# Optimization experiments

Hardware: AMD Instinct MI355X
Metric: run time of the kernel (lower is better)

## Reference

```python
import math
import jax, jax.numpy as jnp
import numpy as np

H = 512   # hidden_size
NH = 8    # num_heads
HD = H // NH  # per_head_size


def get_embedding(max_len, dim):
    # FLAT-style sinusoidal relative position embedding over positions [-L, L-1]
    half = dim // 2
    freq = jnp.exp(jnp.arange(half, dtype=jnp.float32) * (-math.log(10000.0) / (half - 1)))
    pos = jnp.arange(-max_len, max_len, dtype=jnp.float32)  # [2L]
    ang = pos[:, None] * freq[None, :]                      # [2L, half]
    return jnp.concatenate([jnp.sin(ang), jnp.cos(ang)], axis=1)  # [2L, dim]


def setup_inputs() -> dict:
    key = jax.random.key(0)
    ks = jax.random.split(key, 9)
    B, L = 4, 1024
    return {
        "query": jax.random.normal(ks[0], (B, L, H), jnp.float32),
        "key": jax.random.normal(ks[1], (B, L, H), jnp.float32),
        "value": jax.random.normal(ks[2], (B, L, H), jnp.float32),
        "w_q_w": jax.random.normal(ks[3], (H, H), jnp.float32) * 0.02,
        "w_q_b": jnp.zeros((H,), jnp.float32),
        "w_v_w": jax.random.normal(ks[4], (H, H), jnp.float32) * 0.02,
        "w_v_b": jnp.zeros((H,), jnp.float32),
        "w_r_w": jax.random.normal(ks[5], (H, HD), jnp.float32) * 0.02,
        "w_r_b": jnp.zeros((HD,), jnp.float32),
        "r_r_bias": jax.random.normal(ks[6], (NH, HD), jnp.float32) * 0.02,
        "r_w_bias": jax.random.normal(ks[7], (NH, HD), jnp.float32) * 0.02,
        "seq_len": 1000,
    }


def reference(query, key, value, w_q_w, w_q_b, w_v_w, w_v_b, w_r_w, w_r_b,
              r_r_bias, r_w_bias, seq_len):
    B, L, _ = key.shape
    # projections (torch Linear == x @ W + b with W stored as [in, out] here)
    q = (query @ w_q_w + w_q_b).reshape(B, L, NH, HD).transpose(0, 2, 1, 3)  # [B,N,L,D]
    v = (value @ w_v_w + w_v_b).reshape(B, L, NH, HD).transpose(0, 2, 1, 3)
    k = key.reshape(B, L, NH, HD).transpose(0, 2, 1, 3)

    rel = get_embedding(L, H) @ w_r_w + w_r_b  # [2L, HD], positions -L..L-1

    rw_head_q = q + r_r_bias[None, :, None, :]
    AC = jnp.einsum('bnqd,bnkd->bnqk', rw_head_q, k)                 # [B,N,L,L]
    D_ = jnp.einsum('nd,ld->nl', r_w_bias, rel)[None, :, None, :]    # [1,N,1,2L]
    B_ = jnp.einsum('bnqd,ld->bnql', q, rel)                         # [B,N,L,2L]
    E_ = jnp.einsum('bnkd,ld->bnkl', k, rel)                         # [B,N,L,2L]
    BD = B_ + D_

    # _shift:           out[q,k] = BD[q, L + k - q]
    # _transpose_shift: out[q,k] = E_[k, L + q - k]
    qi = jnp.arange(L)
    idx_bd = L + qi[None, :] - qi[:, None]                 # [L,L]: L+k-q
    BD_sh = BD[:, :, qi[:, None], idx_bd]                  # [B,N,L,L]
    rows_e = jnp.broadcast_to(qi[None, :], (L, L))         # [L,L]: k
    idx_e = L + qi[:, None] - qi[None, :]                  # [L,L]: L+q-k
    E_sh = E_[:, :, rows_e, idx_e]                         # [B,N,L,L]

    attn = AC + BD_sh + E_sh
    mask = (jnp.arange(L) < seq_len)[None, None, None, :]  # key mask
    attn = jnp.where(mask, attn, jnp.float32(-1e15))
    attn = jax.nn.softmax(attn, axis=-1)

    out = jnp.matmul(attn, v)                               # [B,N,L,D]
    return out.transpose(0, 2, 1, 3).reshape(B, L, H)
```

## Files before the change

### kernel.cpp

```cpp
#include <hip/hip_runtime.h>
#include <math.h>

#define HDIM  512
#define NHEAD 8
#define HEADD 64
#define BATCH 4
#define SEQ   1024
#define RELN  2048
#define LOG2E 1.4426950408889634f

typedef __attribute__((ext_vector_type(8))) short s16x8;
typedef __attribute__((ext_vector_type(4))) float f32x4;

__device__ __forceinline__ unsigned short f2bf(float x) {
    unsigned u = __float_as_uint(x);
    u += 0x7fffu + ((u >> 16) & 1u);
    return (unsigned short)(u >> 16);
}
__device__ __forceinline__ float bf2f(unsigned short h) {
    return __uint_as_float(((unsigned)h) << 16);
}

__global__ __launch_bounds__(256) void rel_kernel(const float* __restrict__ w_r_w,
                                                  const float* __restrict__ w_r_b,
                                                  unsigned short* __restrict__ relbf)
{
    __shared__ float emb_s[HDIM];
    __shared__ float part[4][64];
    const int l = blockIdx.x;
    const int t = threadIdx.x;
    const float pos  = (float)(l - SEQ);
    const float coef = (float)(-9.210340371976184 / 255.0);
    {
        float fr  = expf((float)t * coef);
        float ang = pos * fr;
        emb_s[t]       = sinf(ang);
        emb_s[t + 256] = cosf(ang);
    }
    __syncthreads();
    const int d  = t & 63;
    const int ks = t >> 6;
    const float* wp = w_r_w + d;
    const int h0 = ks * 128;
    float a0 = 0.f, a1 = 0.f, a2 = 0.f, a3 = 0.f;
    #pragma unroll 8
    for (int h = 0; h < 128; h += 4) {
        a0 = fmaf(emb_s[h0 + h + 0], wp[(size_t)(h0 + h + 0) * HEADD], a0);
        a1 = fmaf(emb_s[h0 + h + 1], wp[(size_t)(h0 + h + 1) * HEADD], a1);
        a2 = fmaf(emb_s[h0 + h + 2], wp[(size_t)(h0 + h + 2) * HEADD], a2);
        a3 = fmaf(emb_s[h0 + h + 3], wp[(size_t)(h0 + h + 3) * HEADD], a3);
    }
    part[ks][d] = (a0 + a1) + (a2 + a3);
    __syncthreads();
    if (ks == 0) {
        float acc = part[0][d] + part[1][d] + part[2][d] + part[3][d] + w_r_b[d];
        relbf[(size_t)l * HEADD + d] = f2bf(acc);
    }
}

__global__ __launch_bounds__(256) void wsplit_kernel(
    const float* __restrict__ wq, const float* __restrict__ wv,
    unsigned short* __restrict__ wtq_hi, unsigned short* __restrict__ wtq_lo,
    unsigned short* __restrict__ wtv_hi, unsigned short* __restrict__ wtv_lo)
{
    __shared__ float T[64][68];
    const float* W = blockIdx.z ? wv : wq;
    unsigned short* Ohi = blockIdx.z ? wtv_hi : wtq_hi;
    unsigned short* Olo = blockIdx.z ? wtv_lo : wtq_lo;
    const int k0 = blockIdx.y * 64, n0 = blockIdx.x * 64;
    const int t = threadIdx.x;
    const int r = t >> 2, c16 = (t & 3) * 16;
    #pragma unroll
    for (int u = 0; u < 4; ++u) {
        float4 v = *(const float4*)(W + (size_t)(k0 + r) * HDIM + n0 + c16 + u * 4);
        *(float4*)&T[r][c16 + u * 4] = v;
    }
    __syncthreads();
    __align__(16) unsigned short hi[16], lo[16];
    #pragma unroll
    for (int u = 0; u < 16; ++u) {
        float x = T[c16 + u][r];
        unsigned short h = f2bf(x);
        hi[u] = h;
        lo[u] = f2bf(x - bf2f(h));
    }
    size_t base = (size_t)(n0 + r) * HDIM + k0 + c16;
    *(uint4*)(Ohi + base)     = *(uint4*)&hi[0];
    *(uint4*)(Ohi + base + 8) = *(uint4*)&hi[8];
    *(uint4*)(Olo + base)     = *(uint4*)&lo[0];
    *(uint4*)(Olo + base + 8) = *(uint4*)&lo[8];
}

__global__ void conv_bf16(const float* __restrict__ in, unsigned short* __restrict__ out, int n)
{
    int i = (blockIdx.x * 256 + threadIdx.x) * 4;
    if (i < n) {
        float4 v = *(const float4*)(in + i);
        ushort4 o;
        o.x = f2bf(v.x); o.y = f2bf(v.y); o.z = f2bf(v.z); o.w = f2bf(v.w);
        *(ushort4*)(out + i) = o;
    }
}

template<int MODE>
__global__ __launch_bounds__(256) void proj_mfma(
    const float* __restrict__ A,
    const unsigned short* __restrict__ Wt_hi,
    const unsigned short* __restrict__ Wt_lo,
    const float* __restrict__ bias,
    const float* __restrict__ e1,
    const float* __restrict__ e2,
    unsigned short* __restrict__ out1,
    unsigned short* __restrict__ out2)
{
    __shared__ unsigned short Ah[64][40], Al[64][40], Bh[64][40], Bl[64][40];
    __shared__ unsigned short Ls[64][72];
    const int t = threadIdx.x;
    const int w = t >> 6, l = t & 63, colA = l & 15, g = l >> 4, kg8 = g * 8;
    const int n0 = blockIdx.x * 64, m0 = blockIdx.y * 64;
    const int mi = w >> 1, ni = w & 1;
    const int sr = t >> 2, skc = (t & 3) * 8;
    f32x4 acc[2][2] = {};

    for (int k0 = 0; k0 < HDIM; k0 += 32) {
        {
            const float* ap = A + (size_t)(m0 + sr) * HDIM + k0 + skc;
            float4 x0 = *(const float4*)ap;
            float4 x1 = *(const float4*)(ap + 4);
            float xv[8] = {x0.x, x0.y, x0.z, x0.w, x1.x, x1.y, x1.z, x1.w};
            __align__(16) unsigned short hh[8], ll[8];
            #pragma unroll
            for (int u = 0; u < 8; ++u) {
                unsigned short h = f2bf(xv[u]);
                hh[u] = h;
                ll[u] = f2bf(xv[u] - bf2f(h));
            }
            *(uint4*)&Ah[sr][skc] = *(uint4*)hh;
            *(uint4*)&Al[sr][skc] = *(uint4*)ll;
            *(uint4*)&Bh[sr][skc] = *(const uint4*)(Wt_hi + (size_t)(n0 + sr) * HDIM + k0 + skc);
            *(uint4*)&Bl[sr][skc] = *(const uint4*)(Wt_lo + (size_t)(n0 + sr) * HDIM + k0 + skc);
        }
        __syncthreads();
        s16x8 ah[2], al[2], bh[2], bl[2];
        #pragma unroll
        for (int mt = 0; mt < 2; ++mt) {
            ah[mt] = *(const s16x8*)&Ah[mi * 32 + mt * 16 + colA][kg8];
            al[mt] = *(const s16x8*)&Al[mi * 32 + mt * 16 + colA][kg8];
        }
        #pragma unroll
        for (int nt = 0; nt < 2; ++nt) {
            bh[nt] = *(const s16x8*)&Bh[ni * 32 + nt * 16 + colA][kg8];
            bl[nt] = *(const s16x8*)&Bl[ni * 32 + nt * 16 + colA][kg8];
        }
        #pragma unroll
        for (int mt = 0; mt < 2; ++mt)
            #pragma unroll
            for (int nt = 0; nt < 2; ++nt) {
                acc[mt][nt] = __builtin_amdgcn_mfma_f32_16x16x32_bf16(al[mt], bh[nt], acc[mt][nt], 0, 0, 0);
                acc[mt][nt] = __builtin_amdgcn_mfma_f32_16x16x32_bf16(ah[mt], bl[nt], acc[mt][nt], 0, 0, 0);
                acc[mt][nt] = __builtin_amdgcn_mfma_f32_16x16x32_bf16(ah[mt], bh[nt], acc[mt][nt], 0, 0, 0);
            }
        __syncthreads();
    }

    float bv[2], ev1[2], ev2[2];
    #pragma unroll
    for (int nt = 0; nt < 2; ++nt) {
        int gn = n0 + ni * 32 + nt * 16 + colA;
        bv[nt] = bias[gn];
        if (MODE == 0) { ev1[nt] = e1[gn]; ev2[nt] = e2[gn]; }
    }

    if (MODE == 0) {
        #pragma unroll
        for (int mt = 0; mt < 2; ++mt)
            #pragma unroll
            for (int nt = 0; nt < 2; ++nt)
                #pragma unroll
                for (int rr = 0; rr < 4; ++rr)
                    Ls[mi * 32 + mt * 16 + g * 4 + rr][ni * 32 + nt * 16 + colA] =
                        f2bf(acc[mt][nt][rr] + bv[nt] + ev1[nt]);
        __syncthreads();
        {
            int r = t >> 2, c = (t & 3) * 16;
            uint4 x0 = *(uint4*)&Ls[r][c];
            uint4 x1 = *(uint4*)&Ls[r][c + 8];
            *(uint4*)(out1 + (size_t)(m0 + r) * HDIM + n0 + c)     = x0;
            *(uint4*)(out1 + (size_t)(m0 + r) * HDIM + n0 + c + 8) = x1;
        }
        __syncthreads();
        #pragma unroll
        for (int mt = 0; mt < 2; ++mt)
            #pragma unroll
            for (int nt = 0; nt < 2; ++nt)
                #pragma unroll
                for (int rr = 0; rr < 4; ++rr)
                    Ls[mi * 32 + mt * 16 + g * 4 + rr][ni * 32 + nt * 16 + colA] =
                        f2bf(acc[mt][nt][rr] + bv[nt] + ev2[nt]);
        __syncthreads();
        {
            int r = t >> 2, c = (t & 3) * 16;
            uint4 x0 = *(uint4*)&Ls[r][c];
            uint4 x1 = *(uint4*)&Ls[r][c + 8];
            *(uint4*)(out2 + (size_t)(m0 + r) * HDIM + n0 + c)     = x0;
            *(uint4*)(out2 + (size_t)(m0 + r) * HDIM + n0 + c + 8) = x1;
        }
    } else {
        #pragma unroll
        for (int mt = 0; mt < 2; ++mt)
            #pragma unroll
            for (int nt = 0; nt < 2; ++nt)
                #pragma unroll
                for (int rr = 0; rr < 4; ++rr)
                    Ls[ni * 32 + nt * 16 + colA][mi * 32 + mt * 16 + g * 4 + rr] =
                        f2bf(acc[mt][nt][rr] + bv[nt]);
        __syncthreads();
        {
            int dl = t >> 2, c = (t & 3) * 16;
            int head = n0 >> 6;
            int bb = m0 >> 10, j0 = m0 & 1023;
            uint4 x0 = *(uint4*)&Ls[dl][c];
            uint4 x1 = *(uint4*)&Ls[dl][c + 8];
            size_t vbase = ((size_t)(bb * NHEAD + head) * HEADD + dl) * SEQ + j0 + c;
            *(uint4*)(out1 + vbase)     = x0;
            *(uint4*)(out1 + vbase + 8) = x1;
        }
    }
}

__global__ __launch_bounds__(256) void flash_v3(
    const unsigned short* __restrict__ kbf,
    const unsigned short* __restrict__ qabf,
    const unsigned short* __restrict__ qbbf,
    const unsigned short* __restrict__ vT,
    const unsigned short* __restrict__ relbf,
    const int* __restrict__ seqp,
    float* __restrict__ out)
{
    __shared__ unsigned short K_s[32][72];
    __shared__ unsigned short Vt_s[64][40];
    __shared__ unsigned short R2_s[64 * 64];
    __shared__ unsigned short R3_s[64 * 64];
    __shared__ unsigned short M2t_s[64][36];
    __shared__ unsigned short M3t_s[64][36];
    __shared__ unsigned short P_s[32][40];
    __shared__ float scale_s[32];
    __shared__ float lsum_s[32];

    const int t = threadIdx.x;
    const int w = t >> 6, l = t & 63, colA = l & 15, g = l >> 4, kg8 = g * 8;
    const int i0 = blockIdx.x * 32;
    const int n = blockIdx.y, b = blockIdx.z;
    const int S = seqp[0];

    const int qa_row = i0 + (w & 1) * 16 + colA;
    const int qb_row = i0 + (w == 3 ? 16 : 0) + colA;
    const s16x8* qaP = (const s16x8*)(qabf + ((size_t)(b * SEQ + qa_row) * HDIM + n * HEADD));
    const s16x8* qbP = (const s16x8*)(qbbf + ((size_t)(b * SEQ + qb_row) * HDIM + n * HEADD));
    const s16x8 qa0 = qaP[g], qa1 = qaP[g + 4];
    const s16x8 qb0 = qbP[g], qb1 = qbP[g + 4];

    float m_run[4] = {-1e30f, -1e30f, -1e30f, -1e30f};
    float l_run[4] = {0.f, 0.f, 0.f, 0.f};
    f32x4 o0 = {0.f, 0.f, 0.f, 0.f}, o1 = {0.f, 0.f, 0.f, 0.f};

    const int krow = t >> 3, kc8 = (t & 7) * 8;
    const int vrow = t >> 2, vc8 = (t & 3) * 8;
    const int orow = (w & 1) * 16;
    const int od   = (w >> 1) * 32;

    for (int j0 = 0; j0 < S; j0 += 32) {
        *(uint4*)&K_s[krow][kc8] =
            *(const uint4*)(kbf + ((size_t)(b * SEQ + j0 + krow) * HDIM + n * HEADD + kc8));
        *(uint4*)&Vt_s[vrow][vc8] =
            *(const uint4*)(vT + ((size_t)((b * NHEAD + n) * HEADD + vrow) * SEQ + j0 + vc8));
        {
            const int base2 = SEQ + j0 - i0 - 31;
            const int base3 = SEQ + i0 - j0 - 31;
            #pragma unroll
            for (int rep = 0; rep < 2; ++rep) {
                int idx = t + rep * 256;
                if (idx < 63 * 8) {
                    int rw = idx >> 3, cc = (idx & 7) * 8;
                    unsigned swz = ((unsigned)(rw * 128 + cc * 2)) ^ (unsigned)((rw & 7) << 4);
                    *(uint4*)((char*)R2_s + swz) =
                        *(const uint4*)(relbf + (size_t)(base2 + rw) * HEADD + cc);
                    *(uint4*)((char*)R3_s + swz) =
                        *(const uint4*)(relbf + (size_t)(base3 + rw) * HEADD + cc);
                }
            }
        }
        __syncthreads();

        f32x4 accS[2] = {};
        if (w < 2) {
            #pragma unroll
            for (int ct = 0; ct < 2; ++ct) {
                s16x8 kb0 = *(const s16x8*)&K_s[ct * 16 + colA][kg8];
                s16x8 kb1 = *(const s16x8*)&K_s[ct * 16 + colA][kg8 + 32];
                accS[ct] = __builtin_amdgcn_mfma_f32_16x16x32_bf16(qa0, kb0, accS[ct], 0, 0, 0);
                accS[ct] = __builtin_amdgcn_mfma_f32_16x16x32_bf16(qa1, kb1, accS[ct], 0, 0, 0);
            }
        } else {
            const int wr = w - 2;
            s16x8 ka0 = *(const s16x8*)&K_s[wr * 16 + colA][kg8];
            s16x8 ka1 = *(const s16x8*)&K_s[wr * 16 + colA][kg8 + 32];
            #pragma unroll
            for (int ut = 0; ut < 4; ++ut) {
                int urow = ut * 16 + colA;
                unsigned sw0 = ((unsigned)(urow * 128 + kg8 * 2)) ^ (unsigned)((urow & 7) << 4);
                unsigned sw1 = ((unsigned)(urow * 128 + (kg8 + 32) * 2)) ^ (unsigned)((urow & 7) << 4);
                s16x8 rb0 = *(const s16x8*)((char*)R2_s + sw0);
                s16x8 rb1 = *(const s16x8*)((char*)R2_s + sw1);
                f32x4 c2 = {};
                c2 = __builtin_amdgcn_mfma_f32_16x16x32_bf16(qb0, rb0, c2, 0, 0, 0);
                c2 = __builtin_amdgcn_mfma_f32_16x16x32_bf16(qb1, rb1, c2, 0, 0, 0);
                ushort4 p2;
                p2.x = f2bf(c2[0]); p2.y = f2bf(c2[1]); p2.z = f2bf(c2[2]); p2.w = f2bf(c2[3]);
                *(ushort4*)&M2t_s[urow][wr * 16 + g * 4] = p2;
                s16x8 sb0 = *(const s16x8*)((char*)R3_s + sw0);
                s16x8 sb1 = *(const s16x8*)((char*)R3_s + sw1);
                f32x4 c3 = {};
                c3 = __builtin_amdgcn_mfma_f32_16x16x32_bf16(ka0, sb0, c3, 0, 0, 0);
                c3 = __builtin_amdgcn_mfma_f32_16x16x32_bf16(ka1, sb1, c3, 0, 0, 0);
                ushort4 p3;
                p3.x = f2bf(c3[0]); p3.y = f2bf(c3[1]); p3.z = f2bf(c3[2]); p3.w = f2bf(c3[3]);
                *(ushort4*)&M3t_s[urow][wr * 16 + g * 4] = p3;
            }
        }
        __syncthreads();

        if (w < 2) {
            float sv[2][4];
            #pragma unroll
            for (int ct = 0; ct < 2; ++ct) {
                int col = ct * 16 + colA;
                bool ok = (j0 + col) < S;
                #pragma unroll
                for (int rr = 0; rr < 4; ++rr) {
                    int grow = orow + g * 4 + rr;
                    float s2 = bf2f(M2t_s[col - grow + 31][grow]);
                    float s3 = bf2f(M3t_s[grow - col + 31][col]);
                    float s = accS[ct][rr] + s2 + s3;
                    sv[ct][rr] = ok ? s : -1e30f;
                }
            }
            #pragma unroll
            for (int rr = 0; rr < 4; ++rr) {
                float mm = fmaxf(sv[0][rr], sv[1][rr]);
                mm = fmaxf(mm, __shfl_xor(mm, 1));
                mm = fmaxf(mm, __shfl_xor(mm, 2));
                mm = fmaxf(mm, __shfl_xor(mm, 4));
                mm = fmaxf(mm, __shfl_xor(mm, 8));
                float mnew = fmaxf(m_run[rr], mm);
                float sc = exp2f((m_run[rr] - mnew) * LOG2E);
                m_run[rr] = mnew;
                float p0 = exp2f((sv[0][rr] - mnew) * LOG2E);
                float p1 = exp2f((sv[1][rr] - mnew) * LOG2E);
                P_s[orow + g * 4 + rr][colA]      = f2bf(p0);
                P_s[orow + g * 4 + rr][16 + colA] = f2bf(p1);
                float pp = p0 + p1;
                pp += __shfl_xor(pp, 1);
                pp += __shfl_xor(pp, 2);
                pp += __shfl_xor(pp, 4);
                pp += __shfl_xor(pp, 8);
                l_run[rr] = l_run[rr] * sc + pp;
                if (colA == 0) scale_s[orow + g * 4 + rr] = sc;
            }
        }
        __syncthreads();

        {
            float s0 = scale_s[orow + g * 4 + 0];
            float s1 = scale_s[orow + g * 4 + 1];
            float s2 = scale_s[orow + g * 4 + 2];
            float s3 = scale_s[orow + g * 4 + 3];
            o0[0] *= s0; o0[1] *= s1; o0[2] *= s2; o0[3] *= s3;
            o1[0] *= s0; o1[1] *= s1; o1[2] *= s2; o1[3] *= s3;
            s16x8 pa  = *(const s16x8*)&P_s[orow + colA][kg8];
            s16x8 vb0 = *(const s16x8*)&Vt_s[od + colA][kg8];
            s16x8 vb1 = *(const s16x8*)&Vt_s[od + 16 + colA][kg8];
            o0 = __builtin_amdgcn_mfma_f32_16x16x32_bf16(pa, vb0, o0, 0, 0, 0);
            o1 = __builtin_amdgcn_mfma_f32_16x16x32_bf16(pa, vb1, o1, 0, 0, 0);
        }
        __syncthreads();
    }

    if (w < 2 && colA == 0) {
        #pragma unroll
        for (int rr = 0; rr < 4; ++rr)
            lsum_s[orow + g * 4 + rr] = l_run[rr];
    }
    __syncthreads();
    #pragma unroll
    for (int rr = 0; rr < 4; ++rr) {
        int row = orow + g * 4 + rr;
        float inv = 1.f / lsum_s[row];
        size_t obase = (size_t)(b * SEQ + i0 + row) * HDIM + n * HEADD;
        out[obase + od + colA]      = o0[rr] * inv;
        out[obase + od + 16 + colA] = o1[rr] * inv;
    }
}

extern "C" void kernel_launch(void* const* d_in, const int* in_sizes, int n_in,
                              void* d_out, int out_size, void* d_ws, size_t ws_size,
                              hipStream_t stream) {
    (void)in_sizes; (void)n_in; (void)out_size; (void)ws_size;
    const float* query = (const float*)d_in[0];
    const float* key   = (const float*)d_in[1];
    const float* value = (const float*)d_in[2];
    const float* w_q_w = (const float*)d_in[3];
    const float* w_q_b = (const float*)d_in[4];
    const float* w_v_w = (const float*)d_in[5];
    const float* w_v_b = (const float*)d_in[6];
    const float* w_r_w = (const float*)d_in[7];
    const float* w_r_b = (const float*)d_in[8];
    const float* rrb   = (const float*)d_in[9];
    const float* rwb   = (const float*)d_in[10];
    const int*   seqp  = (const int*)d_in[11];
    float* out = (float*)d_out;

    unsigned short* wsp   = (unsigned short*)d_ws;
    const size_t NTOK = (size_t)BATCH * SEQ * HDIM;
    unsigned short* relbf  = wsp;
    unsigned short* kbf    = relbf + (size_t)RELN * HEADD;
    unsigned short* qabf   = kbf + NTOK;
    unsigned short* qbbf   = qabf + NTOK;
    unsigned short* vTbuf  = qbbf + NTOK;
    unsigned short* wtq_hi = vTbuf + NTOK;
    unsigned short* wtq_lo = wtq_hi + (size_t)HDIM * HDIM;
    unsigned short* wtv_hi = wtq_lo + (size_t)HDIM * HDIM;
    unsigned short* wtv_lo = wtv_hi + (size_t)HDIM * HDIM;

    hipLaunchKernelGGL(rel_kernel, dim3(RELN), dim3(256), 0, stream, w_r_w, w_r_b, relbf);
    hipLaunchKernelGGL(wsplit_kernel, dim3(8, 8, 2), dim3(256), 0, stream,
                       w_q_w, w_v_w, wtq_hi, wtq_lo, wtv_hi, wtv_lo);
    hipLaunchKernelGGL(conv_bf16, dim3(2048), dim3(256), 0, stream,
                       key, kbf, (int)NTOK);
    hipLaunchKernelGGL((proj_mfma<0>), dim3(8, 64), dim3(256), 0, stream,
                       query, wtq_hi, wtq_lo, w_q_b, rrb, rwb, qabf, qbbf);
    hipLaunchKernelGGL((proj_mfma<1>), dim3(8, 64), dim3(256), 0, stream,
                       value, wtv_hi, wtv_lo, w_v_b, (const float*)nullptr, (const float*)nullptr,
                       vTbuf, (unsigned short*)nullptr);
    hipLaunchKernelGGL(flash_v3, dim3(SEQ / 32, NHEAD, BATCH), dim3(256), 0, stream,
                       kbf, qabf, qbbf, vTbuf, relbf, seqp, out);
}
```

Before: 252.9 us.

## Merge prep kernels, fuse Q/V projections, read relative embeddings directly from global

The three preprocessing kernels (relative embedding, weight hi/lo split, key bf16 conversion) become one launch that dispatches on block index. The Q and V projections become one launch using blockIdx.z. In the flash kernel the shared-memory staging of the relative-embedding slices (R2_s/R3_s) is removed, and the rel-bias waves read relbf rows straight from global/L2 with clamped indices. This cuts launch overhead and shared-memory traffic and footprint, which may raise occupancy, but the flash kernel now issues uncoalesced global loads inside its inner loop.

```diff
diff --git a/kernel.cpp b/kernel.cpp
--- a/kernel.cpp
+++ b/kernel.cpp
@@ -12,6 +12,8 @@
 typedef __attribute__((ext_vector_type(8))) short s16x8;
 typedef __attribute__((ext_vector_type(4))) float f32x4;
 
+#define MFMA __builtin_amdgcn_mfma_f32_16x16x32_bf16
+
 __device__ __forceinline__ unsigned short f2bf(float x) {
     unsigned u = __float_as_uint(x);
     u += 0x7fffu + ((u >> 16) & 1u);
@@ -21,100 +23,106 @@
     return __uint_as_float(((unsigned)h) << 16);
 }
 
-__global__ __launch_bounds__(256) void rel_kernel(const float* __restrict__ w_r_w,
-                                                  const float* __restrict__ w_r_b,
-                                                  unsigned short* __restrict__ relbf)
+__global__ __launch_bounds__(256) void prep_kernel(
+    const float* __restrict__ w_r_w, const float* __restrict__ w_r_b,
+    const float* __restrict__ key,
+    const float* __restrict__ wq, const float* __restrict__ wv,
+    unsigned short* __restrict__ relbf, unsigned short* __restrict__ kbf,
+    unsigned short* __restrict__ wtq_hi, unsigned short* __restrict__ wtq_lo,
+    unsigned short* __restrict__ wtv_hi, unsigned short* __restrict__ wtv_lo)
 {
     __shared__ float emb_s[HDIM];
     __shared__ float part[4][64];
-    const int l = blockIdx.x;
+    __shared__ float T[64][68];
+    const int bid = blockIdx.x;
     const int t = threadIdx.x;
-    const float pos  = (float)(l - SEQ);
-    const float coef = (float)(-9.210340371976184 / 255.0);
-    {
-        float fr  = expf((float)t * coef);
-        float ang = pos * fr;
-        emb_s[t]       = sinf(ang);
-        emb_s[t + 256] = cosf(ang);
-    }
-    __syncthreads();
-    const int d  = t & 63;
-    const int ks = t >> 6;
-    const float* wp = w_r_w + d;
-    const int h0 = ks * 128;
-    float a0 = 0.f, a1 = 0.f, a2 = 0.f, a3 = 0.f;
-    #pragma unroll 8
-    for (int h = 0; h < 128; h += 4) {
-        a0 = fmaf(emb_s[h0 + h + 0], wp[(size_t)(h0 + h + 0) * HEADD], a0);
-        a1 = fmaf(emb_s[h0 + h + 1], wp[(size_t)(h0 + h + 1) * HEADD], a1);
-        a2 = fmaf(emb_s[h0 + h + 2], wp[(size_t)(h0 + h + 2) * HEADD], a2);
-        a3 = fmaf(emb_s[h0 + h + 3], wp[(size_t)(h0 + h + 3) * HEADD], a3);
-    }
-    part[ks][d] = (a0 + a1) + (a2 + a3);
-    __syncthreads();
-    if (ks == 0) {
-        float acc = part[0][d] + part[1][d] + part[2][d] + part[3][d] + w_r_b[d];
-        relbf[(size_t)l * HEADD + d] = f2bf(acc);
-    }
-}
-
-__global__ __launch_bounds__(256) void wsplit_kernel(
-    const float* __restrict__ wq, const float* __restrict__ wv,
-    unsigned short* __restrict__ wtq_hi, unsigned short* __restrict__ wtq_lo,
-    unsigned short* __restrict__ wtv_hi, unsigned short* __restrict__ wtv_lo)
-{
-    __shared__ float T[64][68];
-    const float* W = blockIdx.z ? wv : wq;
-    unsigned short* Ohi = blockIdx.z ? wtv_hi : wtq_hi;
-    unsigned short* Olo = blockIdx.z ? wtv_lo : wtq_lo;
-    const int k0 = blockIdx.y * 64, n0 = blockIdx.x * 64;
-    const int t = threadIdx.x;
-    const int r = t >> 2, c16 = (t & 3) * 16;
-    #pragma unroll
-    for (int u = 0; u < 4; ++u) {
-        float4 v = *(const float4*)(W + (size_t)(k0 + r) * HDIM + n0 + c16 + u * 4);
-        *(float4*)&T[r][c16 + u * 4] = v;
-    }
-    __syncthreads();
-    __align__(16) unsigned short hi[16], lo[16];
-    #pragma unroll
-    for (int u = 0; u < 16; ++u) {
-        float x = T[c16 + u][r];
-        unsigned short h = f2bf(x);
-        hi[u] = h;
-        lo[u] = f2bf(x - bf2f(h));
-    }
-    size_t base = (size_t)(n0 + r) * HDIM + k0 + c16;
-    *(uint4*)(Ohi + base)     = *(uint4*)&hi[0];
-    *(uint4*)(Ohi + base + 8) = *(uint4*)&hi[8];
-    *(uint4*)(Olo + base)     = *(uint4*)&lo[0];
-    *(uint4*)(Olo + base + 8) = *(uint4*)&lo[8];
-}
-
-__global__ void conv_bf16(const float* __restrict__ in, unsigned short* __restrict__ out, int n)
-{
-    int i = (blockIdx.x * 256 + threadIdx.x) * 4;
-    if (i < n) {
-        float4 v = *(const float4*)(in + i);
-        ushort4 o;
-        o.x = f2bf(v.x); o.y = f2bf(v.y); o.z = f2bf(v.z); o.w = f2bf(v.w);
-        *(ushort4*)(out + i) = o;
-    }
-}
-
-template<int MODE>
-__global__ __launch_bounds__(256) void proj_mfma(
-    const float* __restrict__ A,
-    const unsigned short* __restrict__ Wt_hi,
-    const unsigned short* __restrict__ Wt_lo,
-    const float* __restrict__ bias,
-    const float* __restrict__ e1,
-    const float* __restrict__ e2,
-    unsigned short* __restrict__ out1,
-    unsigned short* __restrict__ out2)
+
+    if (bid < RELN) {
+        const int l = bid;
+        const float pos  = (float)(l - SEQ);
+        const float coef = (float)(-9.210340371976184 / 255.0);
+        {
+            float fr  = expf((float)t * coef);
+            float ang = pos * fr;
+            emb_s[t]       = sinf(ang);
+            emb_s[t + 256] = cosf(ang);
+        }
+        __syncthreads();
+        const int d  = t & 63;
+        const int ks = t >> 6;
+        const float* wp = w_r_w + d;
+        const int h0 = ks * 128;
+        float a0 = 0.f, a1 = 0.f, a2 = 0.f, a3 = 0.f;
+        #pragma unroll 8
+        for (int h = 0; h < 128; h += 4) {
+            a0 = fmaf(emb_s[h0 + h + 0], wp[(size_t)(h0 + h + 0) * HEADD], a0);
+            a1 = fmaf(emb_s[h0 + h + 1], wp[(size_t)(h0 + h + 1) * HEADD], a1);
+            a2 = fmaf(emb_s[h0 + h + 2], wp[(size_t)(h0 + h + 2) * HEADD], a2);
+            a3 = fmaf(emb_s[h0 + h + 3], wp[(size_t)(h0 + h + 3) * HEADD], a3);
+        }
+        part[ks][d] = (a0 + a1) + (a2 + a3);
+        __syncthreads();
+        if (ks == 0) {
+            float acc = part[0][d] + part[1][d] + part[2][d] + part[3][d] + w_r_b[d];
+            relbf[(size_t)l * HEADD + d] = f2bf(acc);
+        }
+    } else if (bid < RELN + 128) {
+        const int idx = bid - RELN;
+        const int z = idx >> 6, rem = idx & 63;
+        const int by = rem >> 3, bx = rem & 7;
+        const float* W = z ? wv : wq;
+        unsigned short* Ohi = z ? wtv_hi : wtq_hi;
+        unsigned short* Olo = z ? wtv_lo : wtq_lo;
+        const int k0 = by * 64, n0 = bx * 64;
+        const int r = t >> 2, c16 = (t & 3) * 16;
+        #pragma unroll
+        for (int u = 0; u < 4; ++u) {
+            float4 v = *(const float4*)(W + (size_t)(k0 + r) * HDIM + n0 + c16 + u * 4);
+            *(float4*)&T[r][c16 + u * 4] = v;
+        }
+        __syncthreads();
+        __align__(16) unsigned short hi[16], lo[16];
+        #pragma unroll
+        for (int u = 0; u < 16; ++u) {
+            float x = T[c16 + u][r];
+            unsigned short h = f2bf(x);
+            hi[u] = h;
+            lo[u] = f2bf(x - bf2f(h));
+        }
+        size_t base = (size_t)(n0 + r) * HDIM + k0 + c16;
+        *(uint4*)(Ohi + base)     = *(uint4*)&hi[0];
+        *(uint4*)(Ohi + base + 8) = *(uint4*)&hi[8];
+        *(uint4*)(Olo + base)     = *(uint4*)&lo[0];
+        *(uint4*)(Olo + base + 8) = *(uint4*)&lo[8];
+    } else {
+        const int cid = bid - RELN - 128;
+        const int i = (cid * 256 + t) * 8;
+        float4 v0 = *(const float4*)(key + i);
+        float4 v1 = *(const float4*)(key + i + 4);
+        __align__(16) unsigned short h[8];
+        h[0] = f2bf(v0.x); h[1] = f2bf(v0.y); h[2] = f2bf(v0.z); h[3] = f2bf(v0.w);
+        h[4] = f2bf(v1.x); h[5] = f2bf(v1.y); h[6] = f2bf(v1.z); h[7] = f2bf(v1.w);
+        *(uint4*)(kbf + i) = *(uint4*)h;
+    }
+}
+
+__global__ __launch_bounds__(256) void proj_kernel(
+    const float* __restrict__ query, const float* __restrict__ value,
+    const unsigned short* __restrict__ wtq_hi, const unsigned short* __restrict__ wtq_lo,
+    const unsigned short* __restrict__ wtv_hi, const unsigned short* __restrict__ wtv_lo,
+    const float* __restrict__ w_q_b, const float* __restrict__ w_v_b,
+    const float* __restrict__ rrb, const float* __restrict__ rwb,
+    unsigned short* __restrict__ qabf, unsigned short* __restrict__ qbbf,
+    unsigned short* __restrict__ vTbuf)
 {
     __shared__ unsigned short Ah[64][40], Al[64][40], Bh[64][40], Bl[64][40];
     __shared__ unsigned short Ls[64][72];
+    const int mode = blockIdx.z;
+    const float* A = mode ? value : query;
+    const unsigned short* Wt_hi = mode ? wtv_hi : wtq_hi;
+    const unsigned short* Wt_lo = mode ? wtv_lo : wtq_lo;
+    const float* bias = mode ? w_v_b : w_q_b;
+
     const int t = threadIdx.x;
     const int w = t >> 6, l = t & 63, colA = l & 15, g = l >> 4, kg8 = g * 8;
     const int n0 = blockIdx.x * 64, m0 = blockIdx.y * 64;
@@ -156,9 +164,9 @@
         for (int mt = 0; mt < 2; ++mt)
             #pragma unroll
             for (int nt = 0; nt < 2; ++nt) {
-                acc[mt][nt] = __builtin_amdgcn_mfma_f32_16x16x32_bf16(al[mt], bh[nt], acc[mt][nt], 0, 0, 0);
-                acc[mt][nt] = __builtin_amdgcn_mfma_f32_16x16x32_bf16(ah[mt], bl[nt], acc[mt][nt], 0, 0, 0);
-                acc[mt][nt] = __builtin_amdgcn_mfma_f32_16x16x32_bf16(ah[mt], bh[nt], acc[mt][nt], 0, 0, 0);
+                acc[mt][nt] = MFMA(al[mt], bh[nt], acc[mt][nt], 0, 0, 0);
+                acc[mt][nt] = MFMA(ah[mt], bl[nt], acc[mt][nt], 0, 0, 0);
+                acc[mt][nt] = MFMA(ah[mt], bh[nt], acc[mt][nt], 0, 0, 0);
             }
         __syncthreads();
     }
@@ -168,10 +176,10 @@
     for (int nt = 0; nt < 2; ++nt) {
         int gn = n0 + ni * 32 + nt * 16 + colA;
         bv[nt] = bias[gn];
-        if (MODE == 0) { ev1[nt] = e1[gn]; ev2[nt] = e2[gn]; }
-    }
-
-    if (MODE == 0) {
+        if (mode == 0) { ev1[nt] = rrb[gn]; ev2[nt] = rwb[gn]; }
+    }
+
+    if (mode == 0) {
         #pragma unroll
         for (int mt = 0; mt < 2; ++mt)
             #pragma unroll
@@ -185,8 +193,8 @@
             int r = t >> 2, c = (t & 3) * 16;
             uint4 x0 = *(uint4*)&Ls[r][c];
             uint4 x1 = *(uint4*)&Ls[r][c + 8];
-            *(uint4*)(out1 + (size_t)(m0 + r) * HDIM + n0 + c)     = x0;
-            *(uint4*)(out1 + (size_t)(m0 + r) * HDIM + n0 + c + 8) = x1;
+            *(uint4*)(qabf + (size_t)(m0 + r) * HDIM + n0 + c)     = x0;
+            *(uint4*)(qabf + (size_t)(m0 + r) * HDIM + n0 + c + 8) = x1;
         }
         __syncthreads();
         #pragma unroll
@@ -202,8 +210,8 @@
             int r = t >> 2, c = (t & 3) * 16;
             uint4 x0 = *(uint4*)&Ls[r][c];
             uint4 x1 = *(uint4*)&Ls[r][c + 8];
-            *(uint4*)(out2 + (size_t)(m0 + r) * HDIM + n0 + c)     = x0;
-            *(uint4*)(out2 + (size_t)(m0 + r) * HDIM + n0 + c + 8) = x1;
+            *(uint4*)(qbbf + (size_t)(m0 + r) * HDIM + n0 + c)     = x0;
+            *(uint4*)(qbbf + (size_t)(m0 + r) * HDIM + n0 + c + 8) = x1;
         }
     } else {
         #pragma unroll
@@ -222,8 +230,8 @@
             uint4 x0 = *(uint4*)&Ls[dl][c];
             uint4 x1 = *(uint4*)&Ls[dl][c + 8];
             size_t vbase = ((size_t)(bb * NHEAD + head) * HEADD + dl) * SEQ + j0 + c;
-            *(uint4*)(out1 + vbase)     = x0;
-            *(uint4*)(out1 + vbase + 8) = x1;
+            *(uint4*)(vTbuf + vbase)     = x0;
+            *(uint4*)(vTbuf + vbase + 8) = x1;
         }
     }
 }
@@ -239,8 +247,6 @@
 {
     __shared__ unsigned short K_s[32][72];
     __shared__ unsigned short Vt_s[64][40];
-    __shared__ unsigned short R2_s[64 * 64];
-    __shared__ unsigned short R3_s[64 * 64];
     __shared__ unsigned short M2t_s[64][36];
     __shared__ unsigned short M3t_s[64][36];
     __shared__ unsigned short P_s[32][40];
@@ -274,22 +280,6 @@
             *(const uint4*)(kbf + ((size_t)(b * SEQ + j0 + krow) * HDIM + n * HEADD + kc8));
         *(uint4*)&Vt_s[vrow][vc8] =
             *(const uint4*)(vT + ((size_t)((b * NHEAD + n) * HEADD + vrow) * SEQ + j0 + vc8));
-        {
-            const int base2 = SEQ + j0 - i0 - 31;
-            const int base3 = SEQ + i0 - j0 - 31;
-            #pragma unroll
-            for (int rep = 0; rep < 2; ++rep) {
-                int idx = t + rep * 256;
-                if (idx < 63 * 8) {
-                    int rw = idx >> 3, cc = (idx & 7) * 8;
-                    unsigned swz = ((unsigned)(rw * 128 + cc * 2)) ^ (unsigned)((rw & 7) << 4);
-                    *(uint4*)((char*)R2_s + swz) =
-                        *(const uint4*)(relbf + (size_t)(base2 + rw) * HEADD + cc);
-                    *(uint4*)((char*)R3_s + swz) =
-                        *(const uint4*)(relbf + (size_t)(base3 + rw) * HEADD + cc);
-                }
-            }
-        }
         __syncthreads();
 
         f32x4 accS[2] = {};
@@ -298,31 +288,33 @@
             for (int ct = 0; ct < 2; ++ct) {
                 s16x8 kb0 = *(const s16x8*)&K_s[ct * 16 + colA][kg8];
                 s16x8 kb1 = *(const s16x8*)&K_s[ct * 16 + colA][kg8 + 32];
-                accS[ct] = __builtin_amdgcn_mfma_f32_16x16x32_bf16(qa0, kb0, accS[ct], 0, 0, 0);
-                accS[ct] = __builtin_amdgcn_mfma_f32_16x16x32_bf16(qa1, kb1, accS[ct], 0, 0, 0);
+                accS[ct] = MFMA(qa0, kb0, accS[ct], 0, 0, 0);
+                accS[ct] = MFMA(qa1, kb1, accS[ct], 0, 0, 0);
             }
         } else {
             const int wr = w - 2;
+            const int base2 = SEQ + j0 - i0 - 31;
+            const int base3 = SEQ + i0 - j0 - 31;
             s16x8 ka0 = *(const s16x8*)&K_s[wr * 16 + colA][kg8];
             s16x8 ka1 = *(const s16x8*)&K_s[wr * 16 + colA][kg8 + 32];
             #pragma unroll
             for (int ut = 0; ut < 4; ++ut) {
                 int urow = ut * 16 + colA;
-                unsigned sw0 = ((unsigned)(urow * 128 + kg8 * 2)) ^ (unsigned)((urow & 7) << 4);
-                unsigned sw1 = ((unsigned)(urow * 128 + (kg8 + 32) * 2)) ^ (unsigned)((urow & 7) << 4);
-                s16x8 rb0 = *(const s16x8*)((char*)R2_s + sw0);
-                s16x8 rb1 = *(const s16x8*)((char*)R2_s + sw1);
+                int l2 = base2 + urow; if (l2 > RELN - 1) l2 = RELN - 1;
+                const s16x8* rp2 = (const s16x8*)(relbf + (size_t)l2 * HEADD);
+                s16x8 rb0 = rp2[g], rb1 = rp2[g + 4];
                 f32x4 c2 = {};
-                c2 = __builtin_amdgcn_mfma_f32_16x16x32_bf16(qb0, rb0, c2, 0, 0, 0);
-                c2 = __builtin_amdgcn_mfma_f32_16x16x32_bf16(qb1, rb1, c2, 0, 0, 0);
+                c2 = MFMA(qb0, rb0, c2, 0, 0, 0);
+                c2 = MFMA(qb1, rb1, c2, 0, 0, 0);
                 ushort4 p2;
                 p2.x = f2bf(c2[0]); p2.y = f2bf(c2[1]); p2.z = f2bf(c2[2]); p2.w = f2bf(c2[3]);
                 *(ushort4*)&M2t_s[urow][wr * 16 + g * 4] = p2;
-                s16x8 sb0 = *(const s16x8*)((char*)R3_s + sw0);
-                s16x8 sb1 = *(const s16x8*)((char*)R3_s + sw1);
+                int l3 = base3 + urow; if (l3 > RELN - 1) l3 = RELN - 1;
+                const s16x8* rp3 = (const s16x8*)(relbf + (size_t)l3 * HEADD);
+                s16x8 sb0 = rp3[g], sb1 = rp3[g + 4];
                 f32x4 c3 = {};
-                c3 = __builtin_amdgcn_mfma_f32_16x16x32_bf16(ka0, sb0, c3, 0, 0, 0);
-                c3 = __builtin_amdgcn_mfma_f32_16x16x32_bf16(ka1, sb1, c3, 0, 0, 0);
+                c3 = MFMA(ka0, sb0, c3, 0, 0, 0);
+                c3 = MFMA(ka1, sb1, c3, 0, 0, 0);
                 ushort4 p3;
                 p3.x = f2bf(c3[0]); p3.y = f2bf(c3[1]); p3.z = f2bf(c3[2]); p3.w = f2bf(c3[3]);
                 *(ushort4*)&M3t_s[urow][wr * 16 + g * 4] = p3;
@@ -380,8 +372,8 @@
             s16x8 pa  = *(const s16x8*)&P_s[orow + colA][kg8];
             s16x8 vb0 = *(const s16x8*)&Vt_s[od + colA][kg8];
             s16x8 vb1 = *(const s16x8*)&Vt_s[od + 16 + colA][kg8];
-            o0 = __builtin_amdgcn_mfma_f32_16x16x32_bf16(pa, vb0, o0, 0, 0, 0);
-            o1 = __builtin_amdgcn_mfma_f32_16x16x32_bf16(pa, vb1, o1, 0, 0, 0);
+            o0 = MFMA(pa, vb0, o0, 0, 0, 0);
+            o1 = MFMA(pa, vb1, o1, 0, 0, 0);
         }
         __syncthreads();
     }
@@ -420,7 +412,7 @@
     const int*   seqp  = (const int*)d_in[11];
     float* out = (float*)d_out;
 
-    unsigned short* wsp   = (unsigned short*)d_ws;
+    unsigned short* wsp = (unsigned short*)d_ws;
     const size_t NTOK = (size_t)BATCH * SEQ * HDIM;
     unsigned short* relbf  = wsp;
     unsigned short* kbf    = relbf + (size_t)RELN * HEADD;
@@ -432,16 +424,12 @@
     unsigned short* wtv_hi = wtq_lo + (size_t)HDIM * HDIM;
     unsigned short* wtv_lo = wtv_hi + (size_t)HDIM * HDIM;
 
-    hipLaunchKernelGGL(rel_kernel, dim3(RELN), dim3(256), 0, stream, w_r_w, w_r_b, relbf);
-    hipLaunchKernelGGL(wsplit_kernel, dim3(8, 8, 2), dim3(256), 0, stream,
-                       w_q_w, w_v_w, wtq_hi, wtq_lo, wtv_hi, wtv_lo);
-    hipLaunchKernelGGL(conv_bf16, dim3(2048), dim3(256), 0, stream,
-                       key, kbf, (int)NTOK);
-    hipLaunchKernelGGL((proj_mfma<0>), dim3(8, 64), dim3(256), 0, stream,
-                       query, wtq_hi, wtq_lo, w_q_b, rrb, rwb, qabf, qbbf);
-    hipLaunchKernelGGL((proj_mfma<1>), dim3(8, 64), dim3(256), 0, stream,
-                       value, wtv_hi, wtv_lo, w_v_b, (const float*)nullptr, (const float*)nullptr,
-                       vTbuf, (unsigned short*)nullptr);
+    hipLaunchKernelGGL(prep_kernel, dim3(RELN + 128 + 1024), dim3(256), 0, stream,
+                       w_r_w, w_r_b, key, w_q_w, w_v_w,
+                       relbf, kbf, wtq_hi, wtq_lo, wtv_hi, wtv_lo);
+    hipLaunchKernelGGL(proj_kernel, dim3(8, 64, 2), dim3(256), 0, stream,
+                       query, value, wtq_hi, wtq_lo, wtv_hi, wtv_lo,
+                       w_q_b, w_v_b, rrb, rwb, qabf, qbbf, vTbuf);
     hipLaunchKernelGGL(flash_v3, dim3(SEQ / 32, NHEAD, BATCH), dim3(256), 0, stream,
                        kbf, qabf, qbbf, vTbuf, relbf, seqp, out);
 }
```

New measurement: 282.8 us. +11.8%, slower.
